# Kernel tuning notes

Measured on AMD Instinct MI355X. Metric: run time of the kernel, lower is better.

Reference implementation:

```python
import jax, jax.numpy as jnp
import numpy as np

D_MODEL = 768
D_POS = 64
NHEAD = 12
D_FF = 3072
HEAD_DIM = D_MODEL // NHEAD
LN_EPS = 1e-5


def _layer_norm(x, gamma, beta):
    mu = jnp.mean(x, axis=-1, keepdims=True)
    var = jnp.var(x, axis=-1, keepdims=True)
    return (x - mu) * jax.lax.rsqrt(var + LN_EPS) * gamma + beta


def setup_inputs() -> dict:
    key = jax.random.key(0)
    ks = jax.random.split(key, 16)
    L, N = 256, 4
    s = 0.02
    return {
        "src": jax.random.normal(ks[0], (L, N, D_MODEL), jnp.float32),
        "pos": jax.random.normal(ks[1], (N, L, L, D_POS), jnp.float32),
        "q_w": jax.random.normal(ks[2], (D_MODEL, D_MODEL), jnp.float32) * s,
        "q_b": jnp.zeros((D_MODEL,), jnp.float32),
        "k_w": jax.random.normal(ks[3], (D_MODEL, D_MODEL), jnp.float32) * s,
        "k_b": jnp.zeros((D_MODEL,), jnp.float32),
        "v_w": jax.random.normal(ks[4], (D_MODEL, D_MODEL), jnp.float32) * s,
        "v_b": jnp.zeros((D_MODEL,), jnp.float32),
        "p_w": jax.random.normal(ks[5], (D_MODEL, D_POS), jnp.float32) * s,
        "p_b": jnp.zeros((D_MODEL,), jnp.float32),
        "out_w": jax.random.normal(ks[6], (D_MODEL, D_MODEL), jnp.float32) * s,
        "out_b": jnp.zeros((D_MODEL,), jnp.float32),
        "lin1_w": jax.random.normal(ks[7], (D_FF, D_MODEL), jnp.float32) * s,
        "lin1_b": jnp.zeros((D_FF,), jnp.float32),
        "lin2_w": jax.random.normal(ks[8], (D_MODEL, D_FF), jnp.float32) * s,
        "lin2_b": jnp.zeros((D_MODEL,), jnp.float32),
        "n1_g": jnp.ones((D_MODEL,), jnp.float32),
        "n1_b": jnp.zeros((D_MODEL,), jnp.float32),
        "n2_g": jnp.ones((D_MODEL,), jnp.float32),
        "n2_b": jnp.zeros((D_MODEL,), jnp.float32),
    }


def reference(src, pos, q_w, q_b, k_w, k_b, v_w, v_b, p_w, p_b,
              out_w, out_b, lin1_w, lin1_b, lin2_w, lin2_b,
              n1_g, n1_b, n2_g, n2_b):
    L, N, E = src.shape
    H, hd = NHEAD, HEAD_DIM
    scaling = float(hd) ** -0.5

    # projections (F.linear: x @ W.T + b)
    q = (src @ q_w.T + q_b).reshape(L, N, H, hd).transpose(1, 2, 0, 3) * scaling  # (N,H,L,hd)
    k = (src @ k_w.T + k_b).reshape(L, N, H, hd).transpose(1, 2, 0, 3)            # (N,H,L,hd)
    v = (src @ v_w.T + v_b).reshape(L, N, H, hd).transpose(1, 2, 0, 3)            # (N,H,L,hd)
    p = (pos @ p_w.T + p_b).reshape(N, L, L, H, hd)                               # (N,L,L,H,hd)

    # content-content + content-position scores
    scores = jnp.einsum('nhid,nhjd->nhij', q, k) \
           + jnp.einsum('nhid,nijhd->nhij', q, p)                                 # (N,H,L,L)
    attn = jax.nn.softmax(scores, axis=-1)

    ctx = jnp.einsum('nhij,nhjd->nhid', attn, v)          # (N,H,L,hd)
    ctx = ctx.transpose(2, 0, 1, 3).reshape(L, N, E)      # (L,N,E)
    attn_out = ctx @ out_w.T + out_b

    x = _layer_norm(src + attn_out, n1_g, n1_b)
    ff = jax.nn.gelu(x @ lin1_w.T + lin1_b, approximate=False) @ lin2_w.T + lin2_b
    x = _layer_norm(x + ff, n2_g, n2_b)
    return x
```

## Files before the change

### kernel.cpp

```cpp
#include <hip/hip_runtime.h>
#include <hip/hip_bf16.h>
#include <math.h>

typedef __hip_bfloat16 bf16;
typedef unsigned short u16;
typedef __attribute__((ext_vector_type(8))) short bf16x8;
typedef __attribute__((ext_vector_type(4))) float f32x4;

#define L_SEQ 256
#define NB 4
#define EMB 768
#define NH 12
#define DFF 3072
#define HD 64

__device__ __forceinline__ float ldE(const void* p, size_t i, int f32) {
    return f32 ? ((const float*)p)[i] : __bfloat162float(((const bf16*)p)[i]);
}
__device__ __forceinline__ float b2f(u16 v) { return __uint_as_float(((unsigned)v) << 16); }
__device__ __forceinline__ u16 f2b(float v) {
    bf16 h = __float2bfloat16(v);
    return *(u16*)&h;
}

__device__ __forceinline__ void cvt8(u16* dst, const void* s, size_t off, int f32) {
    if (f32) {
        const float* sf = (const float*)s + off;
        #pragma unroll
        for (int t = 0; t < 8; ++t) dst[t] = f2b(sf[t]);
    } else {
        *(uint4*)dst = *(const uint4*)((const u16*)s + off);
    }
}

__device__ __forceinline__ int detect_flag(const void* src, int* lds4) {
    int t = threadIdx.x;
    int wave = t >> 6, lane = t & 63;
    unsigned w = ((const unsigned*)src)[t];
    unsigned e = ((w & 0xFFFFu) >> 7) & 0xFFu;
    unsigned long long m = __ballot(e >= 0xC3u);
    if (lane == 0) lds4[wave] = __popcll(m);
    __syncthreads();
    return (lds4[0] + lds4[1] + lds4[2] + lds4[3]) > 8 ? 1 : 0;
}

__global__ void pack_all(u16* __restrict__ xb, u16* __restrict__ wqkv,
                         u16* __restrict__ owb, u16* __restrict__ l1b,
                         u16* __restrict__ l2b, float* __restrict__ biasf,
                         const void* src, const void* qw, const void* kw, const void* vw,
                         const void* ow, const void* l1w, const void* l2w,
                         const void* qb, const void* kb, const void* vb,
                         const void* ob, const void* b1, const void* b2,
                         int* __restrict__ flagp) {
    __shared__ int lds4[4];
    const int f32 = detect_flag(src, lds4);
    int b = blockIdx.x;
    if (b == 0 && threadIdx.x == 0) *flagp = f32;
    if (b >= 3840) {
        int o = (b - 3840) * 256 + threadIdx.x;
        if (o >= 6912) return;
        float v;
        if (o < 768)       v = ldE(qb, o, f32);
        else if (o < 1536) v = ldE(kb, o - 768, f32);
        else if (o < 2304) v = ldE(vb, o - 1536, f32);
        else if (o < 3072) v = ldE(ob, o - 2304, f32);
        else if (o < 6144) v = ldE(b1, o - 3072, f32);
        else               v = ldE(b2, o - 6144, f32);
        biasf[o] = v;
        return;
    }
    int gid = b * 256 + threadIdx.x;
    u16 tmp[8];
    if (gid < 98304) {
        size_t idx = (size_t)gid * 8;
        cvt8(tmp, src, idx, f32);
        *(uint4*)(xb + idx) = *(uint4*)tmp;
    } else if (gid < 319488) {
        size_t idx = (size_t)(gid - 98304) * 8;
        int r = (int)(idx / EMB);
        const void* s;
        size_t off;
        if (r < EMB)          { s = qw; off = idx; }
        else if (r < 2 * EMB) { s = kw; off = idx - (size_t)EMB * EMB; }
        else                  { s = vw; off = idx - (size_t)2 * EMB * EMB; }
        cvt8(tmp, s, off, f32);
        *(uint4*)(wqkv + idx) = *(uint4*)tmp;
    } else if (gid < 393216) {
        size_t idx = (size_t)(gid - 319488) * 8;
        cvt8(tmp, ow, idx, f32);
        *(uint4*)(owb + idx) = *(uint4*)tmp;
    } else if (gid < 688128) {
        size_t idx = (size_t)(gid - 393216) * 8;
        cvt8(tmp, l1w, idx, f32);
        *(uint4*)(l1b + idx) = *(uint4*)tmp;
    } else {
        size_t idx = (size_t)(gid - 688128) * 8;
        cvt8(tmp, l2w, idx, f32);
        *(uint4*)(l2b + idx) = *(uint4*)tmp;
    }
}

template <int MODE>
__global__ __launch_bounds__(256, 2) void mfma_gemm(
        const u16* __restrict__ A, const u16* __restrict__ W,
        const float* __restrict__ biasf,
        u16* __restrict__ outB0, u16* __restrict__ outB1, u16* __restrict__ outB2,
        float* __restrict__ outF, float* __restrict__ outF2,
        int K, int lda, int ksplit) {
    __shared__ u16 As[64][32];
    __shared__ u16 Ws[128][32];
    int tid = threadIdx.x;
    int wave = tid >> 6, lane = tid & 63;
    int quad = lane >> 4, col = lane & 15;
    int m0 = blockIdx.y * 64, n0 = blockIdx.x * 128;
    int z = blockIdx.z;
    const u16* Ap = A + (size_t)z * ksplit;
    const u16* Wp = W + (size_t)z * ksplit;
    int wm = (wave >> 1) * 32, wn = (wave & 1) * 64;
    f32x4 acc[2][4];
    #pragma unroll
    for (int a = 0; a < 2; ++a)
        #pragma unroll
        for (int b = 0; b < 4; ++b) acc[a][b] = (f32x4){0.f, 0.f, 0.f, 0.f};
    for (int k0 = 0; k0 < K; k0 += 32) {
        {
            int r = tid >> 2, c4 = (tid & 3) * 8;
            const u16* ga = &Ap[(size_t)(m0 + r) * lda + k0 + c4];
            unsigned off = (unsigned)(wave * 64 * 16);
            __builtin_amdgcn_global_load_lds(
                (const __attribute__((address_space(1))) void*)ga,
                (__attribute__((address_space(3))) void*)((char*)&As[0][0] + off),
                16, 0, 0);
        }
        #pragma unroll
        for (int it = 0; it < 2; ++it) {
            int l = tid + it * 256;
            int r = l >> 2, c4 = (l & 3) * 8;
            const u16* gw = &Wp[(size_t)(n0 + r) * lda + k0 + c4];
            unsigned off = (unsigned)((it * 256 + wave * 64) * 16);
            __builtin_amdgcn_global_load_lds(
                (const __attribute__((address_space(1))) void*)gw,
                (__attribute__((address_space(3))) void*)((char*)&Ws[0][0] + off),
                16, 0, 0);
        }
        __syncthreads();
        bf16x8 af[2], bfr[4];
        #pragma unroll
        for (int mi = 0; mi < 2; ++mi)
            af[mi] = __builtin_bit_cast(bf16x8, *(const uint4*)&As[wm + mi * 16 + col][quad * 8]);
        #pragma unroll
        for (int ni = 0; ni < 4; ++ni)
            bfr[ni] = __builtin_bit_cast(bf16x8, *(const uint4*)&Ws[wn + ni * 16 + col][quad * 8]);
        #pragma unroll
        for (int mi = 0; mi < 2; ++mi)
            #pragma unroll
            for (int ni = 0; ni < 4; ++ni)
                acc[mi][ni] = __builtin_amdgcn_mfma_f32_16x16x32_bf16(
                    af[mi], bfr[ni], acc[mi][ni], 0, 0, 0);
        __syncthreads();
    }
    #pragma unroll
    for (int mi = 0; mi < 2; ++mi)
        #pragma unroll
        for (int ni = 0; ni < 4; ++ni)
            #pragma unroll
            for (int reg = 0; reg < 4; ++reg) {
                int rr = m0 + wm + mi * 16 + quad * 4 + reg;
                int cc = n0 + wn + ni * 16 + col;
                float v = acc[mi][ni][reg];
                if (MODE == 0) {
                    v += biasf[cc];
                    int i = rr >> 2, n = rr & 3;
                    if (cc < EMB) {
                        int h = cc >> 6, d = cc & 63;
                        outB0[(((size_t)(n * NH + h)) * L_SEQ + i) * HD + d] = f2b(v * 0.125f);
                    } else if (cc < 2 * EMB) {
                        int c2 = cc - EMB;
                        int h = c2 >> 6, d = c2 & 63;
                        outB1[(((size_t)(n * NH + h)) * L_SEQ + i) * HD + d] = f2b(v);
                    } else {
                        outB2[((size_t)n * EMB + (cc - 2 * EMB)) * L_SEQ + i] = f2b(v);
                    }
                } else if (MODE == 2) {
                    v += biasf[cc];
                    v = 0.5f * v * (1.0f + erff(v * 0.70710678118654752f));
                    outB0[(size_t)rr * DFF + cc] = f2b(v);
                } else if (MODE == 4) {
                    float* o = z ? outF2 : outF;
                    o[(size_t)rr * EMB + cc] = v;
                } else {
                    atomicAdd(&outF[(size_t)rr * EMB + cc], v);
                }
            }
}

__global__ __launch_bounds__(256) void qp_kernel(
        const u16* __restrict__ qb, const void* __restrict__ p_w,
        const void* __restrict__ p_b, u16* __restrict__ qp_b,
        float* __restrict__ qpb, const int* __restrict__ flagp) {
    const int f32 = *flagp;
    int w = threadIdx.x >> 6, t = threadIdx.x & 63;
    int blk = blockIdx.x * 4 + w;
    int i = blk & 255;
    int h = (blk >> 8) % NH;
    int n = blk / (256 * NH);
    __shared__ float qs[4][64];
    qs[w][t] = b2f(qb[(((size_t)(n * NH + h)) * L_SEQ + i) * HD + t]);
    __syncthreads();
    float acc = 0.f;
    #pragma unroll 16
    for (int d = 0; d < 64; ++d)
        acc += qs[w][d] * ldE(p_w, (size_t)(h * HD + d) * HD + t, f32);
    qp_b[(((size_t)(n * L_SEQ + i)) * 16 + h) * 64 + t] = f2b(acc);
    float v = qs[w][t] * ldE(p_b, h * HD + t, f32);
    #pragma unroll
    for (int off = 32; off; off >>= 1) v += __shfl_down(v, off);
    if (t == 0) qpb[blk] = v;
}

__global__ __launch_bounds__(64) void s2_mfma(
        const u16* __restrict__ qp_b, const float* __restrict__ qpb,
        const void* __restrict__ pos, float* __restrict__ S,
        const int* __restrict__ flagp) {
    const int f32 = *flagp;
    int wid = blockIdx.x;
    int jh = blockIdx.y;
    int i = wid & 255, n = wid >> 8;
    int lane = threadIdx.x;
    int quad = lane >> 4, col = lane & 15;
    const u16* qprow = qp_b + (((size_t)wid) * 16 + col) * 64;
    bf16x8 a0 = __builtin_bit_cast(bf16x8, *(const uint4*)(qprow + quad * 8));
    bf16x8 a1 = __builtin_bit_cast(bf16x8, *(const uint4*)(qprow + 32 + quad * 8));
    float qpb_r[4];
    #pragma unroll
    for (int reg = 0; reg < 4; ++reg) {
        int h = quad * 4 + reg;
        qpb_r[reg] = (h < NH) ? qpb[((size_t)n * NH + h) * L_SEQ + i] : 0.f;
    }
    #pragma unroll
    for (int tt = 0; tt < 4; ++tt) {
        int t = jh * 4 + tt;
        int j = t * 16 + col;
        size_t pbase = ((size_t)(n * L_SEQ + i) * L_SEQ + j) * HD;
        bf16x8 b0, b1;
        if (f32) {
            const float* pf = (const float*)pos + pbase;
            u16 tmp[16];
            #pragma unroll
            for (int c = 0; c < 8; ++c) tmp[c] = f2b(pf[quad * 8 + c]);
            #pragma unroll
            for (int c = 0; c < 8; ++c) tmp[8 + c] = f2b(pf[32 + quad * 8 + c]);
            b0 = *(bf16x8*)tmp;
            b1 = *(bf16x8*)(tmp + 8);
        } else {
            const u16* pb = (const u16*)pos + pbase;
            b0 = __builtin_bit_cast(bf16x8, *(const uint4*)(pb + quad * 8));
            b1 = __builtin_bit_cast(bf16x8, *(const uint4*)(pb + 32 + quad * 8));
        }
        f32x4 acc = (f32x4){0.f, 0.f, 0.f, 0.f};
        acc = __builtin_amdgcn_mfma_f32_16x16x32_bf16(a0, b0, acc, 0, 0, 0);
        acc = __builtin_amdgcn_mfma_f32_16x16x32_bf16(a1, b1, acc, 0, 0, 0);
        if (quad < 3) {
            #pragma unroll
            for (int reg = 0; reg < 4; ++reg) {
                int h = quad * 4 + reg;
                S[(((size_t)n * NH + h) * L_SEQ + i) * L_SEQ + j] = acc[reg] + qpb_r[reg];
            }
        }
    }
}

__global__ __launch_bounds__(64) void attn3_kernel(
        const u16* __restrict__ qb, const u16* __restrict__ kb,
        const u16* __restrict__ vt, const float* __restrict__ S,
        u16* __restrict__ ctxb) {
    __shared__ u16 p_lds[16][268];
    int b = blockIdx.x;
    int n = b / (NH * 16), rem = b % (NH * 16), h = rem >> 4, it = rem & 15;
    int lane = threadIdx.x;
    int quad = lane >> 4, col = lane & 15;
    int i0 = it * 16;

    const u16* qh = qb + ((size_t)(n * NH + h)) * L_SEQ * HD;
    const u16* kh = kb + ((size_t)(n * NH + h)) * L_SEQ * HD;

    const u16* qrow = qh + (size_t)(i0 + col) * HD;
    bf16x8 a0 = __builtin_bit_cast(bf16x8, *(const uint4*)(qrow + quad * 8));
    bf16x8 a1 = __builtin_bit_cast(bf16x8, *(const uint4*)(qrow + 32 + quad * 8));

    f32x4 sc[16];
    #pragma unroll
    for (int t = 0; t < 16; ++t) {
        const u16* krow = kh + (size_t)(t * 16 + col) * HD;
        bf16x8 b0 = __builtin_bit_cast(bf16x8, *(const uint4*)(krow + quad * 8));
        bf16x8 b1 = __builtin_bit_cast(bf16x8, *(const uint4*)(krow + 32 + quad * 8));
        f32x4 acc = (f32x4){0.f, 0.f, 0.f, 0.f};
        acc = __builtin_amdgcn_mfma_f32_16x16x32_bf16(a0, b0, acc, 0, 0, 0);
        acc = __builtin_amdgcn_mfma_f32_16x16x32_bf16(a1, b1, acc, 0, 0, 0);
        sc[t] = acc;
    }

    #pragma unroll
    for (int reg = 0; reg < 4; ++reg) {
        const float* Srow = S + (((size_t)n * NH + h) * L_SEQ + i0 + quad * 4 + reg) * L_SEQ + col;
        float m = -1e30f;
        #pragma unroll
        for (int t = 0; t < 16; ++t) {
            float v = sc[t][reg] + Srow[t * 16];
            sc[t][reg] = v;
            m = fmaxf(m, v);
        }
        #pragma unroll
        for (int off = 1; off < 16; off <<= 1) m = fmaxf(m, __shfl_xor(m, off));
        float sum = 0.f;
        #pragma unroll
        for (int t = 0; t < 16; ++t) {
            float e = __expf(sc[t][reg] - m);
            sc[t][reg] = e;
            sum += e;
        }
        #pragma unroll
        for (int off = 1; off < 16; off <<= 1) sum += __shfl_xor(sum, off);
        float inv = 1.0f / sum;
        #pragma unroll
        for (int t = 0; t < 16; ++t)
            p_lds[quad * 4 + reg][t * 16 + col] = f2b(sc[t][reg] * inv);
    }

    bf16x8 ap[8];
    #pragma unroll
    for (int kt = 0; kt < 8; ++kt)
        ap[kt] = __builtin_bit_cast(bf16x8, *(const uint4*)&p_lds[col][kt * 32 + quad * 8]);
    #pragma unroll
    for (int nt = 0; nt < 4; ++nt) {
        const u16* vrow = vt + ((size_t)n * EMB + h * HD + nt * 16 + col) * L_SEQ;
        f32x4 acc = (f32x4){0.f, 0.f, 0.f, 0.f};
        #pragma unroll
        for (int kt = 0; kt < 8; ++kt) {
            bf16x8 bp = __builtin_bit_cast(bf16x8, *(const uint4*)(vrow + kt * 32 + quad * 8));
            acc = __builtin_amdgcn_mfma_f32_16x16x32_bf16(ap[kt], bp, acc, 0, 0, 0);
        }
        #pragma unroll
        for (int reg = 0; reg < 4; ++reg) {
            int ii = i0 + quad * 4 + reg;
            ctxb[((size_t)ii * NB + n) * EMB + h * HD + nt * 16 + col] = f2b(acc[reg]);
        }
    }
}

__device__ __forceinline__ float blk_sum(float v, volatile float* ws, int wave, int lane) {
    #pragma unroll
    for (int off = 32; off; off >>= 1) v += __shfl_xor(v, off);
    if (lane == 0) ws[wave] = v;
    __syncthreads();
    float s = ws[0] + ws[1] + ws[2] + ws[3];
    __syncthreads();
    return s;
}

__global__ void ln1_kernel(const float* __restrict__ p0, const float* __restrict__ p1,
                           const void* __restrict__ src, const float* __restrict__ biasf,
                           const void* __restrict__ g, const void* __restrict__ b,
                           u16* __restrict__ x1b, float* __restrict__ y2,
                           const int* __restrict__ flagp) {
    const int f32 = *flagp;
    int r = blockIdx.x;
    int t = threadIdx.x;
    int wave = t >> 6, lane = t & 63;
    __shared__ float ws[4];
    float x[3];
    #pragma unroll
    for (int p = 0; p < 3; ++p) {
        int e = t + p * 256;
        size_t oi = (size_t)r * EMB + e;
        x[p] = p0[oi] + p1[oi] + ldE(src, oi, f32) + biasf[2304 + e];
    }
    float mean = blk_sum(x[0] + x[1] + x[2], ws, wave, lane) * (1.0f / EMB);
    float d0 = x[0] - mean, d1 = x[1] - mean, d2 = x[2] - mean;
    float var = blk_sum(d0 * d0 + d1 * d1 + d2 * d2, ws, wave, lane) * (1.0f / EMB);
    float rstd = rsqrtf(var + 1e-5f);
    float vs[3] = {d0, d1, d2};
    #pragma unroll
    for (int p = 0; p < 3; ++p) {
        int e = t + p * 256;
        float v = vs[p] * rstd * ldE(g, e, f32) + ldE(b, e, f32);
        size_t oi = (size_t)r * EMB + e;
        x1b[oi] = f2b(v);
        y2[oi] = v + biasf[6144 + e];
    }
}

__global__ void ln2_kernel(const float* __restrict__ X, const void* __restrict__ g,
                           const void* __restrict__ b, void* __restrict__ outAny,
                           const int* __restrict__ flagp) {
    const int f32 = *flagp;
    int r = blockIdx.x;
    int t = threadIdx.x;
    int wave = t >> 6, lane = t & 63;
    __shared__ float ws[4];
    float x0 = X[(size_t)r * EMB + t];
    float x1 = X[(size_t)r * EMB + t + 256];
    float x2 = X[(size_t)r * EMB + t + 512];
    float mean = blk_sum(x0 + x1 + x2, ws, wave, lane) * (1.0f / EMB);
    float d0 = x0 - mean, d1 = x1 - mean, d2 = x2 - mean;
    float var = blk_sum(d0 * d0 + d1 * d1 + d2 * d2, ws, wave, lane) * (1.0f / EMB);
    float rstd = rsqrtf(var + 1e-5f);
    float vs[3] = {d0, d1, d2};
    #pragma unroll
    for (int p = 0; p < 3; ++p) {
        int e = t + p * 256;
        float v = vs[p] * rstd * ldE(g, e, f32) + ldE(b, e, f32);
        size_t oi = (size_t)r * EMB + e;
        if (f32) ((float*)outAny)[oi] = v;
        else     ((bf16*)outAny)[oi] = __float2bfloat16(v);
    }
}

extern "C" void kernel_launch(void* const* d_in, const int* in_sizes, int n_in,
                              void* d_out, int out_size, void* d_ws, size_t ws_size,
                              hipStream_t stream) {
    const void* src    = d_in[0];
    const void* pos    = d_in[1];
    const void* q_w    = d_in[2];
    const void* q_b    = d_in[3];
    const void* k_w    = d_in[4];
    const void* k_b    = d_in[5];
    const void* v_w    = d_in[6];
    const void* v_b    = d_in[7];
    const void* p_w    = d_in[8];
    const void* p_b    = d_in[9];
    const void* out_w  = d_in[10];
    const void* out_b  = d_in[11];
    const void* lin1_w = d_in[12];
    const void* lin1_b = d_in[13];
    const void* lin2_w = d_in[14];
    const void* lin2_b = d_in[15];
    const void* n1_g   = d_in[16];
    const void* n1_b   = d_in[17];
    const void* n2_g   = d_in[18];
    const void* n2_b   = d_in[19];

    float* f = (float*)d_ws;
    int*   flagp = (int*)f;
    float* biasf = f + 16;
    u16*   xb    = (u16*)(f + 6928);
    u16*   wqkv  = (u16*)(f + 400144);
    u16*   owb   = (u16*)(f + 1284880);
    u16*   l1b   = (u16*)(f + 1579792);
    u16*   l2b   = (u16*)(f + 2759440);
    u16*   qbp   = (u16*)(f + 3939088);
    u16*   kbp   = (u16*)(f + 4332304);
    u16*   vtb   = (u16*)(f + 4725520);
    u16*   qp_b  = (u16*)(f + 5118736);
    float* qpb   = f + 5643024;
    float* S     = f + 5655312;
    u16*   ctxb  = (u16*)(f + 8801040);
    u16*   ffb   = (u16*)S;
    float* y2    = S + 1572864;
    float* pOut1 = S + 2359296;
    float* pOut0 = f + 400144;
    u16*   x1b   = vtb;

    pack_all<<<3867, 256, 0, stream>>>(xb, wqkv, owb, l1b, l2b, biasf,
                                       src, q_w, k_w, v_w, out_w, lin1_w, lin2_w,
                                       q_b, k_b, v_b, out_b, lin1_b, lin2_b, flagp);

    mfma_gemm<0><<<dim3(18, 16), 256, 0, stream>>>(
        xb, wqkv, biasf, qbp, kbp, vtb, nullptr, nullptr, EMB, EMB, 0);

    qp_kernel<<<NB * NH * L_SEQ / 4, 256, 0, stream>>>(qbp, p_w, p_b, qp_b, qpb, flagp);
    s2_mfma<<<dim3(NB * L_SEQ, 4), 64, 0, stream>>>(qp_b, qpb, pos, S, flagp);

    attn3_kernel<<<NB * NH * 16, 64, 0, stream>>>(qbp, kbp, vtb, S, ctxb);

    mfma_gemm<4><<<dim3(6, 16, 2), 256, 0, stream>>>(
        ctxb, owb, nullptr, nullptr, nullptr, nullptr, pOut0, pOut1, 384, EMB, 384);

    ln1_kernel<<<1024, 256, 0, stream>>>(pOut0, pOut1, src, biasf, n1_g, n1_b,
                                         x1b, y2, flagp);

    mfma_gemm<2><<<dim3(24, 16), 256, 0, stream>>>(
        x1b, l1b, biasf + 3072, ffb, nullptr, nullptr, nullptr, nullptr, EMB, EMB, 0);

    mfma_gemm<5><<<dim3(6, 16, 4), 256, 0, stream>>>(
        ffb, l2b, nullptr, nullptr, nullptr, nullptr, y2, nullptr, 768, DFF, 768);

    ln2_kernel<<<1024, 256, 0, stream>>>(y2, n2_g, n2_b, d_out, flagp);
}
```

Measured before the change: 279.1 us.

## Split attention block work across four waves with cross-wave softmax reduction

The attention kernel now runs 256 threads per block instead of one wave. Each wave computes a quarter of the key tiles for QK^T and one 16-column slice of the PV output. Row max and sum are combined across waves through shared memory with extra barriers. This raises parallelism and cuts per-thread register use in a kernel that launched only 768 single-wave blocks, at the cost of three block-level syncs.

Result: faster. 270.4 us (-3.1%).

```diff
diff --git a/kernel.cpp b/kernel.cpp
--- a/kernel.cpp
+++ b/kernel.cpp
@@ -270,14 +270,16 @@
     }
 }
 
-__global__ __launch_bounds__(64) void attn3_kernel(
+__global__ __launch_bounds__(256) void attn3_kernel(
         const u16* __restrict__ qb, const u16* __restrict__ kb,
         const u16* __restrict__ vt, const float* __restrict__ S,
         u16* __restrict__ ctxb) {
     __shared__ u16 p_lds[16][268];
+    __shared__ float lds_m[4][16];
+    __shared__ float lds_s[4][16];
     int b = blockIdx.x;
     int n = b / (NH * 16), rem = b % (NH * 16), h = rem >> 4, it = rem & 15;
-    int lane = threadIdx.x;
+    int wave = threadIdx.x >> 6, lane = threadIdx.x & 63;
     int quad = lane >> 4, col = lane & 15;
     int i0 = it * 16;
 
@@ -288,16 +290,17 @@
     bf16x8 a0 = __builtin_bit_cast(bf16x8, *(const uint4*)(qrow + quad * 8));
     bf16x8 a1 = __builtin_bit_cast(bf16x8, *(const uint4*)(qrow + 32 + quad * 8));
 
-    f32x4 sc[16];
-    #pragma unroll
-    for (int t = 0; t < 16; ++t) {
+    f32x4 sc[4];
+    #pragma unroll
+    for (int tt = 0; tt < 4; ++tt) {
+        int t = wave * 4 + tt;
         const u16* krow = kh + (size_t)(t * 16 + col) * HD;
         bf16x8 b0 = __builtin_bit_cast(bf16x8, *(const uint4*)(krow + quad * 8));
         bf16x8 b1 = __builtin_bit_cast(bf16x8, *(const uint4*)(krow + 32 + quad * 8));
         f32x4 acc = (f32x4){0.f, 0.f, 0.f, 0.f};
         acc = __builtin_amdgcn_mfma_f32_16x16x32_bf16(a0, b0, acc, 0, 0, 0);
         acc = __builtin_amdgcn_mfma_f32_16x16x32_bf16(a1, b1, acc, 0, 0, 0);
-        sc[t] = acc;
+        sc[tt] = acc;
     }
 
     #pragma unroll
@@ -305,35 +308,54 @@
         const float* Srow = S + (((size_t)n * NH + h) * L_SEQ + i0 + quad * 4 + reg) * L_SEQ + col;
         float m = -1e30f;
         #pragma unroll
-        for (int t = 0; t < 16; ++t) {
-            float v = sc[t][reg] + Srow[t * 16];
-            sc[t][reg] = v;
+        for (int tt = 0; tt < 4; ++tt) {
+            float v = sc[tt][reg] + Srow[(wave * 4 + tt) * 16];
+            sc[tt][reg] = v;
             m = fmaxf(m, v);
         }
         #pragma unroll
         for (int off = 1; off < 16; off <<= 1) m = fmaxf(m, __shfl_xor(m, off));
+        if (col == 0) lds_m[wave][quad * 4 + reg] = m;
+    }
+    __syncthreads();
+    float gm[4];
+    #pragma unroll
+    for (int reg = 0; reg < 4; ++reg) {
+        int row = quad * 4 + reg;
+        gm[reg] = fmaxf(fmaxf(lds_m[0][row], lds_m[1][row]),
+                        fmaxf(lds_m[2][row], lds_m[3][row]));
+    }
+    #pragma unroll
+    for (int reg = 0; reg < 4; ++reg) {
         float sum = 0.f;
         #pragma unroll
-        for (int t = 0; t < 16; ++t) {
-            float e = __expf(sc[t][reg] - m);
-            sc[t][reg] = e;
+        for (int tt = 0; tt < 4; ++tt) {
+            float e = __expf(sc[tt][reg] - gm[reg]);
+            sc[tt][reg] = e;
             sum += e;
         }
         #pragma unroll
         for (int off = 1; off < 16; off <<= 1) sum += __shfl_xor(sum, off);
-        float inv = 1.0f / sum;
-        #pragma unroll
-        for (int t = 0; t < 16; ++t)
-            p_lds[quad * 4 + reg][t * 16 + col] = f2b(sc[t][reg] * inv);
-    }
+        if (col == 0) lds_s[wave][quad * 4 + reg] = sum;
+    }
+    __syncthreads();
+    #pragma unroll
+    for (int reg = 0; reg < 4; ++reg) {
+        int row = quad * 4 + reg;
+        float gs = lds_s[0][row] + lds_s[1][row] + lds_s[2][row] + lds_s[3][row];
+        float inv = 1.0f / gs;
+        #pragma unroll
+        for (int tt = 0; tt < 4; ++tt)
+            p_lds[row][(wave * 4 + tt) * 16 + col] = f2b(sc[tt][reg] * inv);
+    }
+    __syncthreads();
 
     bf16x8 ap[8];
     #pragma unroll
     for (int kt = 0; kt < 8; ++kt)
         ap[kt] = __builtin_bit_cast(bf16x8, *(const uint4*)&p_lds[col][kt * 32 + quad * 8]);
-    #pragma unroll
-    for (int nt = 0; nt < 4; ++nt) {
-        const u16* vrow = vt + ((size_t)n * EMB + h * HD + nt * 16 + col) * L_SEQ;
+    {
+        const u16* vrow = vt + ((size_t)n * EMB + h * HD + wave * 16 + col) * L_SEQ;
         f32x4 acc = (f32x4){0.f, 0.f, 0.f, 0.f};
         #pragma unroll
         for (int kt = 0; kt < 8; ++kt) {
@@ -343,7 +365,7 @@
         #pragma unroll
         for (int reg = 0; reg < 4; ++reg) {
             int ii = i0 + quad * 4 + reg;
-            ctxb[((size_t)ii * NB + n) * EMB + h * HD + nt * 16 + col] = f2b(acc[reg]);
+            ctxb[((size_t)ii * NB + n) * EMB + h * HD + wave * 16 + col] = f2b(acc[reg]);
         }
     }
 }
@@ -471,7 +493,7 @@
     qp_kernel<<<NB * NH * L_SEQ / 4, 256, 0, stream>>>(qbp, p_w, p_b, qp_b, qpb, flagp);
     s2_mfma<<<dim3(NB * L_SEQ, 4), 64, 0, stream>>>(qp_b, qpb, pos, S, flagp);
 
-    attn3_kernel<<<NB * NH * 16, 64, 0, stream>>>(qbp, kbp, vtb, S, ctxb);
+    attn3_kernel<<<NB * NH * 16, 256, 0, stream>>>(qbp, kbp, vtb, S, ctxb);
 
     mfma_gemm<4><<<dim3(6, 16, 2), 256, 0, stream>>>(
         ctxb, owb, nullptr, nullptr, nullptr, nullptr, pOut0, pOut1, 384, EMB, 384);
```
